# Kernel optimization log

Measured on AMD Instinct MI355X. Metric: run time of the kernel, lower is better.

Reference implementation:

```python
import jax, jax.numpy as jnp
import numpy as np

EPS = 1e-9

def setup_inputs() -> dict:
    key = jax.random.key(0)
    k1, k2 = jax.random.split(key)
    N, K, D = 65536, 512, 768
    return {
        "embeddings": jax.random.normal(k1, (N, D), dtype=jnp.float32),
        "cluster_centers": jax.random.normal(k2, (K, D), dtype=jnp.float32),
        "alpha": 1.0,
    }


def reference(embeddings, cluster_centers, alpha):
    # Student-t soft assignment (DEC): q_ik = (1 + ||x_i - c_k||^2 / alpha)^(-(alpha+1)/2), row-normalized.
    # Squared distance via expansion to avoid materializing the [N, K, D] broadcast:
    x_sq = jnp.sum(embeddings * embeddings, axis=1, keepdims=True)          # [N, 1]
    c_sq = jnp.sum(cluster_centers * cluster_centers, axis=1)               # [K]
    cross = jnp.einsum("nd,kd->nk", embeddings, cluster_centers)            # [N, K]
    norm_squared = jnp.maximum(x_sq - 2.0 * cross + c_sq[None, :], 0.0)     # [N, K]
    numerator = 1.0 / (1.0 + norm_squared / alpha)
    power = (alpha + 1.0) / 2.0
    numerator = numerator ** power
    cluster_p = numerator / jnp.sum(numerator, axis=1, keepdims=True)       # [N, K]
    return cluster_p
```

## Files before the change

### kernel.cpp

```cpp
#include <hip/hip_runtime.h>
#include <hip/hip_bf16.h>

#define D_DIM 768
#define K_CL  512
#define BM    128
#define BK    32
#define NSTEP 24

using f32x4 = __attribute__((ext_vector_type(4))) float;
using s16x8 = __attribute__((ext_vector_type(8))) short;
using u16x8 = __attribute__((ext_vector_type(8))) unsigned short;
using u16x4 = __attribute__((ext_vector_type(4))) unsigned short;

static __device__ __forceinline__ unsigned short f2bf(float f) {
    __hip_bfloat16 h = __float2bfloat16(f);
    unsigned short u;
    __builtin_memcpy(&u, &h, 2);
    return u;
}

__global__ void prep_centers_kernel(const float* __restrict__ C,
                                    unsigned short* __restrict__ Cbws,
                                    float* __restrict__ csq) {
    const int r = blockIdx.x;
    const int l = threadIdx.x;
    const float* src = C + (size_t)r * D_DIM;
    float sq = 0.f;
#pragma unroll
    for (int jj = 0; jj < 2; ++jj) {
        const int j = l + jj * 64;
        if (j < 96) {
            const int t = j >> 2, s = j & 3;
            const int k0 = t * 32 + s * 8;
            f32x4 v0 = *reinterpret_cast<const f32x4*>(src + k0);
            f32x4 v1 = *reinterpret_cast<const f32x4*>(src + k0 + 4);
            u16x8 b;
            b[0] = f2bf(v0[0]); b[1] = f2bf(v0[1]); b[2] = f2bf(v0[2]); b[3] = f2bf(v0[3]);
            b[4] = f2bf(v1[0]); b[5] = f2bf(v1[1]); b[6] = f2bf(v1[2]); b[7] = f2bf(v1[3]);
            sq += v0[0]*v0[0] + v0[1]*v0[1] + v0[2]*v0[2] + v0[3]*v0[3]
                + v1[0]*v1[0] + v1[1]*v1[1] + v1[2]*v1[2] + v1[3]*v1[3];
            const int g = t * 2048 + (r >> 6) * 256 + ((r >> 4) & 3) * 64
                        + s * 16 + (r & 15);
            *reinterpret_cast<u16x8*>(Cbws + (size_t)g * 8) = b;
        }
    }
#pragma unroll
    for (int m = 1; m < 64; m <<= 1) sq += __shfl_xor(sq, m, 64);
    if (l == 0) csq[r] = sq;
}

__global__ __launch_bounds__(1024, 4) void dec_main_kernel(
    const float* __restrict__ X,
    const unsigned short* __restrict__ Cbws,
    const float* __restrict__ csq,
    const float* __restrict__ alpha_ptr,
    float* __restrict__ out)
{
    __shared__ unsigned short Al[2][BM * BK];
    __shared__ float part[8][BM];
    __shared__ float xsql[BM];
    __shared__ float invl[BM];

    const int tid  = threadIdx.x;
    const int lane = tid & 63;
    const int wid  = tid >> 6;
    const int wm   = wid >> 3;
    const int wn   = wid & 7;
    const int m0   = blockIdx.x * BM;

    const int arow  = tid >> 3;
    const int acol8 = tid & 7;
    const float* aptr = X + (size_t)(m0 + arow) * D_DIM + acol8 * 4;
    const int awbyte = arow * 64
                     + ((((acol8 >> 1) ^ ((arow >> 1) & 3))) << 4)
                     + (acol8 & 1) * 8;

    const int fr = lane & 15;
    const int fg = lane >> 4;
    const int abase = wm * 4096 + fr * 64 + ((fg ^ ((fr >> 1) & 3)) << 4);

    const unsigned short* bptr = Cbws + (size_t)(wn * 256 + lane) * 8;

    f32x4 acc[4][4] = {};
    s16x8 bA[4];
    float sqp = 0.f;

    f32x4 areg = *reinterpret_cast<const f32x4*>(aptr);
#pragma unroll
    for (int nf = 0; nf < 4; ++nf)
        bA[nf] = *reinterpret_cast<const s16x8*>(bptr + nf * 512);
    {
        u16x4 ab;
        ab[0] = f2bf(areg[0]); ab[1] = f2bf(areg[1]);
        ab[2] = f2bf(areg[2]); ab[3] = f2bf(areg[3]);
        sqp += areg[0]*areg[0] + areg[1]*areg[1] + areg[2]*areg[2] + areg[3]*areg[3];
        *reinterpret_cast<u16x4*>((char*)&Al[0][0] + awbyte) = ab;
    }
    areg = *reinterpret_cast<const f32x4*>(aptr + BK);
    asm volatile("s_waitcnt lgkmcnt(0)" ::: "memory");
    __builtin_amdgcn_sched_barrier(0);
    __builtin_amdgcn_s_barrier();

    for (int t = 0; t < NSTEP; ++t) {
        {
            const char* ab = (const char*)&Al[t & 1][0] + abase;
            s16x8 afr[4];
#pragma unroll
            for (int mf = 0; mf < 4; ++mf)
                afr[mf] = *reinterpret_cast<const s16x8*>(ab + mf * 1024);
            __builtin_amdgcn_s_setprio(1);
#pragma unroll
            for (int nf = 0; nf < 4; ++nf) {
#pragma unroll
                for (int mf = 0; mf < 4; ++mf)
                    acc[mf][nf] = __builtin_amdgcn_mfma_f32_16x16x32_bf16(
                        afr[mf], bA[nf], acc[mf][nf], 0, 0, 0);
            }
            __builtin_amdgcn_s_setprio(0);
        }
        if (t + 1 < NSTEP) {
            const unsigned short* bp = bptr + (size_t)(t + 1) * 16384;
#pragma unroll
            for (int nf = 0; nf < 4; ++nf)
                bA[nf] = *reinterpret_cast<const s16x8*>(bp + nf * 512);
            u16x4 ab;
            ab[0] = f2bf(areg[0]); ab[1] = f2bf(areg[1]);
            ab[2] = f2bf(areg[2]); ab[3] = f2bf(areg[3]);
            sqp += areg[0]*areg[0] + areg[1]*areg[1] + areg[2]*areg[2] + areg[3]*areg[3];
            *reinterpret_cast<u16x4*>((char*)&Al[(t + 1) & 1][0] + awbyte) = ab;
            if (t + 2 < NSTEP)
                areg = *reinterpret_cast<const f32x4*>(aptr + (t + 2) * BK);
            asm volatile("s_waitcnt lgkmcnt(0)" ::: "memory");
            __builtin_amdgcn_sched_barrier(0);
            __builtin_amdgcn_s_barrier();
        }
    }

    sqp += __shfl_xor(sqp, 1, 64);
    sqp += __shfl_xor(sqp, 2, 64);
    sqp += __shfl_xor(sqp, 4, 64);
    if ((tid & 7) == 0) xsql[arow] = sqp;
    __syncthreads();

    const float alpha     = alpha_ptr[0];
    const float inv_alpha = 1.0f / alpha;
    const float power     = 0.5f * (alpha + 1.0f);
    const bool  p1        = (power == 1.0f);

    float csqr[4];
#pragma unroll
    for (int nf = 0; nf < 4; ++nf)
        csqr[nf] = csq[wn * 64 + nf * 16 + fr];

    if (p1) {
#pragma unroll
        for (int mf = 0; mf < 4; ++mf) {
#pragma unroll
            for (int j = 0; j < 4; ++j) {
                const int rloc = wm * 64 + mf * 16 + fg * 4 + j;
                const float xs = xsql[rloc];
                float rp = 0.f;
#pragma unroll
                for (int nf = 0; nf < 4; ++nf) {
                    float d2 = xs + csqr[nf] - 2.0f * acc[mf][nf][j];
                    d2 = fmaxf(d2, 0.0f);
                    const float nm = 1.0f / (1.0f + d2 * inv_alpha);
                    acc[mf][nf][j] = nm;
                    rp += nm;
                }
#pragma unroll
                for (int m = 1; m < 16; m <<= 1) rp += __shfl_xor(rp, m, 64);
                if (fr == 0) part[wn][rloc] = rp;
            }
        }
    } else {
#pragma unroll
        for (int mf = 0; mf < 4; ++mf) {
#pragma unroll
            for (int j = 0; j < 4; ++j) {
                const int rloc = wm * 64 + mf * 16 + fg * 4 + j;
                const float xs = xsql[rloc];
                float rp = 0.f;
#pragma unroll
                for (int nf = 0; nf < 4; ++nf) {
                    float d2 = xs + csqr[nf] - 2.0f * acc[mf][nf][j];
                    d2 = fmaxf(d2, 0.0f);
                    const float base = 1.0f + d2 * inv_alpha;
                    const float nm = exp2f(-power * log2f(base));
                    acc[mf][nf][j] = nm;
                    rp += nm;
                }
#pragma unroll
                for (int m = 1; m < 16; m <<= 1) rp += __shfl_xor(rp, m, 64);
                if (fr == 0) part[wn][rloc] = rp;
            }
        }
    }
    __syncthreads();
    if (tid < BM) {
        float s = 0.f;
#pragma unroll
        for (int w = 0; w < 8; ++w) s += part[w][tid];
        invl[tid] = 1.0f / s;
    }
    __syncthreads();

#pragma unroll
    for (int mf = 0; mf < 4; ++mf) {
#pragma unroll
        for (int j = 0; j < 4; ++j) {
            const int rloc = wm * 64 + mf * 16 + fg * 4 + j;
            const float iv = invl[rloc];
            float* orow = out + (size_t)(m0 + rloc) * K_CL + wn * 64 + fr;
#pragma unroll
            for (int nf = 0; nf < 4; ++nf)
                orow[nf * 16] = acc[mf][nf][j] * iv;
        }
    }
}

extern "C" void kernel_launch(void* const* d_in, const int* in_sizes, int n_in,
                              void* d_out, int out_size, void* d_ws, size_t ws_size,
                              hipStream_t stream) {
    const float* X     = (const float*)d_in[0];
    const float* C     = (const float*)d_in[1];
    const float* alpha = (const float*)d_in[2];
    float* out = (float*)d_out;
    const int N = in_sizes[0] / D_DIM;

    unsigned short* Cbws = (unsigned short*)d_ws;
    float* csq = (float*)((char*)d_ws + (size_t)K_CL * D_DIM * sizeof(unsigned short));

    prep_centers_kernel<<<K_CL, 64, 0, stream>>>(C, Cbws, csq);
    dec_main_kernel<<<N / BM, 1024, 0, stream>>>(X, Cbws, csq, alpha, out);
}
```

Before: 137.7 us.

## Shrink row tile to 64 with 512-thread blocks and stage three k-slices per barrier

Row tile per block drops from 128 to 64 and the block from 1024 to 512 threads, with each of the 8 waves owning one 64-column slice. Each LDS stage now holds three 32-wide k slices (96 columns), so there are 8 barriers instead of 24, while B fragments are still reloaded from global per 32-wide slice. The aim is fewer block-wide syncs and smaller blocks that schedule more flexibly. In exchange the centers operand is reloaded for twice as many blocks, which adds L2 traffic.

```diff
diff --git a/kernel.cpp b/kernel.cpp
--- a/kernel.cpp
+++ b/kernel.cpp
@@ -3,9 +3,9 @@
 
 #define D_DIM 768
 #define K_CL  512
-#define BM    128
-#define BK    32
-#define NSTEP 24
+#define BM    64
+#define BK    96
+#define NSTEP 8
 
 using f32x4 = __attribute__((ext_vector_type(4))) float;
 using s16x8 = __attribute__((ext_vector_type(8))) short;
@@ -49,7 +49,7 @@
     if (l == 0) csq[r] = sq;
 }
 
-__global__ __launch_bounds__(1024, 4) void dec_main_kernel(
+__global__ __launch_bounds__(512, 4) void dec_main_kernel(
     const float* __restrict__ X,
     const unsigned short* __restrict__ Cbws,
     const float* __restrict__ csq,
@@ -63,9 +63,7 @@
 
     const int tid  = threadIdx.x;
     const int lane = tid & 63;
-    const int wid  = tid >> 6;
-    const int wm   = wid >> 3;
-    const int wn   = wid & 7;
+    const int wn   = tid >> 6;
     const int m0   = blockIdx.x * BM;
 
     const int arow  = tid >> 3;
@@ -77,7 +75,7 @@
 
     const int fr = lane & 15;
     const int fg = lane >> 4;
-    const int abase = wm * 4096 + fr * 64 + ((fg ^ ((fr >> 1) & 3)) << 4);
+    const int abase = fr * 64 + ((fg ^ ((fr >> 1) & 3)) << 4);
 
     const unsigned short* bptr = Cbws + (size_t)(wn * 256 + lane) * 8;
 
@@ -85,29 +83,42 @@
     s16x8 bA[4];
     float sqp = 0.f;
 
-    f32x4 areg = *reinterpret_cast<const f32x4*>(aptr);
+#define STAGE_A(ar, dstbase, kk)                                               \
+    {                                                                          \
+        u16x4 ab_;                                                             \
+        ab_[0] = f2bf((ar)[0]); ab_[1] = f2bf((ar)[1]);                        \
+        ab_[2] = f2bf((ar)[2]); ab_[3] = f2bf((ar)[3]);                        \
+        sqp += (ar)[0]*(ar)[0] + (ar)[1]*(ar)[1]                               \
+             + (ar)[2]*(ar)[2] + (ar)[3]*(ar)[3];                              \
+        *reinterpret_cast<u16x4*>((dstbase) + (kk) * 4096 + awbyte) = ab_;     \
+    }
+
+    f32x4 ar0 = *reinterpret_cast<const f32x4*>(aptr);
+    f32x4 ar1 = *reinterpret_cast<const f32x4*>(aptr + 32);
+    f32x4 ar2 = *reinterpret_cast<const f32x4*>(aptr + 64);
 #pragma unroll
     for (int nf = 0; nf < 4; ++nf)
         bA[nf] = *reinterpret_cast<const s16x8*>(bptr + nf * 512);
     {
-        u16x4 ab;
-        ab[0] = f2bf(areg[0]); ab[1] = f2bf(areg[1]);
-        ab[2] = f2bf(areg[2]); ab[3] = f2bf(areg[3]);
-        sqp += areg[0]*areg[0] + areg[1]*areg[1] + areg[2]*areg[2] + areg[3]*areg[3];
-        *reinterpret_cast<u16x4*>((char*)&Al[0][0] + awbyte) = ab;
-    }
-    areg = *reinterpret_cast<const f32x4*>(aptr + BK);
+        char* dst = (char*)&Al[0][0];
+        STAGE_A(ar0, dst, 0); STAGE_A(ar1, dst, 1); STAGE_A(ar2, dst, 2);
+    }
+    ar0 = *reinterpret_cast<const f32x4*>(aptr + BK);
+    ar1 = *reinterpret_cast<const f32x4*>(aptr + BK + 32);
+    ar2 = *reinterpret_cast<const f32x4*>(aptr + BK + 64);
     asm volatile("s_waitcnt lgkmcnt(0)" ::: "memory");
     __builtin_amdgcn_sched_barrier(0);
     __builtin_amdgcn_s_barrier();
 
-    for (int t = 0; t < NSTEP; ++t) {
-        {
-            const char* ab = (const char*)&Al[t & 1][0] + abase;
+    for (int T = 0; T < NSTEP; ++T) {
+        const char* abuf = (const char*)&Al[T & 1][0];
+#pragma unroll
+        for (int kk = 0; kk < 3; ++kk) {
             s16x8 afr[4];
 #pragma unroll
             for (int mf = 0; mf < 4; ++mf)
-                afr[mf] = *reinterpret_cast<const s16x8*>(ab + mf * 1024);
+                afr[mf] = *reinterpret_cast<const s16x8*>(
+                    abuf + kk * 4096 + abase + mf * 1024);
             __builtin_amdgcn_s_setprio(1);
 #pragma unroll
             for (int nf = 0; nf < 4; ++nf) {
@@ -117,24 +128,29 @@
                         afr[mf], bA[nf], acc[mf][nf], 0, 0, 0);
             }
             __builtin_amdgcn_s_setprio(0);
-        }
-        if (t + 1 < NSTEP) {
-            const unsigned short* bp = bptr + (size_t)(t + 1) * 16384;
-#pragma unroll
-            for (int nf = 0; nf < 4; ++nf)
-                bA[nf] = *reinterpret_cast<const s16x8*>(bp + nf * 512);
-            u16x4 ab;
-            ab[0] = f2bf(areg[0]); ab[1] = f2bf(areg[1]);
-            ab[2] = f2bf(areg[2]); ab[3] = f2bf(areg[3]);
-            sqp += areg[0]*areg[0] + areg[1]*areg[1] + areg[2]*areg[2] + areg[3]*areg[3];
-            *reinterpret_cast<u16x4*>((char*)&Al[(t + 1) & 1][0] + awbyte) = ab;
-            if (t + 2 < NSTEP)
-                areg = *reinterpret_cast<const f32x4*>(aptr + (t + 2) * BK);
+            const int tn = T * 3 + kk + 1;
+            if (tn < 24) {
+                const unsigned short* bp = bptr + (size_t)tn * 16384;
+#pragma unroll
+                for (int nf = 0; nf < 4; ++nf)
+                    bA[nf] = *reinterpret_cast<const s16x8*>(bp + nf * 512);
+            }
+        }
+        if (T + 1 < NSTEP) {
+            char* dst = (char*)&Al[(T + 1) & 1][0];
+            STAGE_A(ar0, dst, 0); STAGE_A(ar1, dst, 1); STAGE_A(ar2, dst, 2);
+            if (T + 2 < NSTEP) {
+                const float* ap = aptr + (T + 2) * BK;
+                ar0 = *reinterpret_cast<const f32x4*>(ap);
+                ar1 = *reinterpret_cast<const f32x4*>(ap + 32);
+                ar2 = *reinterpret_cast<const f32x4*>(ap + 64);
+            }
             asm volatile("s_waitcnt lgkmcnt(0)" ::: "memory");
             __builtin_amdgcn_sched_barrier(0);
             __builtin_amdgcn_s_barrier();
         }
     }
+#undef STAGE_A
 
     sqp += __shfl_xor(sqp, 1, 64);
     sqp += __shfl_xor(sqp, 2, 64);
@@ -157,7 +173,7 @@
         for (int mf = 0; mf < 4; ++mf) {
 #pragma unroll
             for (int j = 0; j < 4; ++j) {
-                const int rloc = wm * 64 + mf * 16 + fg * 4 + j;
+                const int rloc = mf * 16 + fg * 4 + j;
                 const float xs = xsql[rloc];
                 float rp = 0.f;
 #pragma unroll
@@ -178,7 +194,7 @@
         for (int mf = 0; mf < 4; ++mf) {
 #pragma unroll
             for (int j = 0; j < 4; ++j) {
-                const int rloc = wm * 64 + mf * 16 + fg * 4 + j;
+                const int rloc = mf * 16 + fg * 4 + j;
                 const float xs = xsql[rloc];
                 float rp = 0.f;
 #pragma unroll
@@ -209,7 +225,7 @@
     for (int mf = 0; mf < 4; ++mf) {
 #pragma unroll
         for (int j = 0; j < 4; ++j) {
-            const int rloc = wm * 64 + mf * 16 + fg * 4 + j;
+            const int rloc = mf * 16 + fg * 4 + j;
             const float iv = invl[rloc];
             float* orow = out + (size_t)(m0 + rloc) * K_CL + wn * 64 + fr;
 #pragma unroll
@@ -232,5 +248,5 @@
     float* csq = (float*)((char*)d_ws + (size_t)K_CL * D_DIM * sizeof(unsigned short));
 
     prep_centers_kernel<<<K_CL, 64, 0, stream>>>(C, Cbws, csq);
-    dec_main_kernel<<<N / BM, 1024, 0, stream>>>(X, Cbws, csq, alpha, out);
-}
+    dec_main_kernel<<<N / BM, 512, 0, stream>>>(X, Cbws, csq, alpha, out);
+}
```

Measured after the change: 138.6 us. Within noise of the previous version (+0.6%).
